# Kernel optimization log

Measured on AMD Instinct MI355X. Metric: run time of the kernel, lower is better.

Reference implementation:

```python
import jax, jax.numpy as jnp
import numpy as np
import math

FILTER_SIZE = 11
FILTER_SIGMA = 1.5
C1 = 0.01 ** 2
C2 = 0.03 ** 2
PAD = FILTER_SIZE // 2


def _make_gauss_kernel(sigma, kernel_size, channel=3):
    mean = np.floor(0.5 * kernel_size)
    x = np.arange(kernel_size, dtype=np.float64)
    k1d = np.exp(-((x - mean) ** 2) / (2 * sigma ** 2)) * (1.0 / (2 * math.pi * sigma ** 2))
    k2d = np.outer(k1d, k1d).astype(np.float32)
    k2d = k2d / k2d.sum()
    # OIHW depthwise kernel: [channel, 1, k, k]
    return np.broadcast_to(k2d[None, None], (channel, 1, kernel_size, kernel_size)).copy()


def _depthwise_blur(x, kernel):
    # x: [B, 3, H, W], kernel: [3, 1, k, k]; groups=3, SAME padding (k//2)
    return jax.lax.conv_general_dilated(
        x, kernel,
        window_strides=(1, 1),
        padding=[(PAD, PAD), (PAD, PAD)],
        dimension_numbers=('NCHW', 'OIHW', 'NCHW'),
        feature_group_count=3,
    )


def setup_inputs() -> dict:
    key = jax.random.key(0)
    k1, k2 = jax.random.split(key)
    B, C, H, W = 32, 3, 512, 512
    image1 = jax.random.uniform(k1, (B, C, H, W), dtype=jnp.float32)
    image2 = jax.random.uniform(k2, (B, C, H, W), dtype=jnp.float32)
    gauss_kernel = jnp.asarray(_make_gauss_kernel(FILTER_SIGMA, FILTER_SIZE, channel=3))
    return {"image1": image1, "image2": image2, "gauss_kernel": gauss_kernel}


def reference(image1, image2, gauss_kernel):
    mu1 = _depthwise_blur(image1, gauss_kernel)
    mu2 = _depthwise_blur(image2, gauss_kernel)
    mu1_sq = mu1 * mu1
    mu2_sq = mu2 * mu2
    mu1_mu2 = mu1 * mu2
    sig1_sq = _depthwise_blur(image1 * image1, gauss_kernel) - mu1_sq
    sig2_sq = _depthwise_blur(image2 * image2, gauss_kernel) - mu2_sq
    sig1_sig2 = _depthwise_blur(image1 * image2, gauss_kernel) - mu1_mu2
    ssim_num = (2.0 * mu1_mu2 + C1) * (2.0 * sig1_sig2 + C2)
    ssim_den = (mu1_sq + mu2_sq + C1) * (sig1_sq + sig2_sq + C2)
    ssim_map = ssim_num / ssim_den
    dssim_map = (1.0 - ssim_map) * 0.5
    return dssim_map.mean()  # size_average=True
```

## Files before the change

### kernel.cpp

```cpp
#include <hip/hip_runtime.h>
#include <math.h>


namespace {
constexpr int IMG = 512;
constexpr int TW = 32;
constexpr int RB = 64;
constexpr int RING = RB + 10;
constexpr int SLOT = 44;
constexpr int XGN = TW / 8;
constexpr int NCHUNK = IMG / RB;
constexpr int CTILES = IMG / TW;
constexpr int NIMG = 96;
constexpr float C1c = 1e-4f;
constexpr float C2c = 9e-4f;
constexpr float INV_N = 1.0f / 25165824.0f;
}

typedef float v2f __attribute__((ext_vector_type(2)));

__global__ void dssim_zero(float* ws) { ws[0] = 0.0f; }

__global__ void dssim_final(const float* __restrict__ ws, float* __restrict__ out) {
  out[0] = ws[0] * INV_N;
}

__global__ __launch_bounds__(256, 3) void dssim_main(
    const float* __restrict__ im1, const float* __restrict__ im2,
    const float* __restrict__ gk, float* __restrict__ ws)
{
  __shared__ float sR[XGN * RING * SLOT];

  const int tid = threadIdx.x;
  const int bid = blockIdx.x;
  const int img = bid >> 4;
  const int tsx = bid & 15;
  const int X0s = tsx * TW;

  const float* __restrict__ p1 = im1 + (size_t)img * (IMG * IMG);
  const float* __restrict__ p2 = im2 + (size_t)img * (IMG * IMG);

  float wt[11];
  {
    float ic = 1.0f / sqrtf(gk[5 * 11 + 5]);
    #pragma unroll
    for (int i = 0; i < 11; ++i) wt[i] = gk[i * 11 + 5] * ic;
  }
  v2f wp[12];
  #pragma unroll
  for (int m = 0; m < 12; ++m) {
    float lo = (m <= 10) ? wt[m] : 0.f;
    float hi = (m >= 1) ? wt[m - 1] : 0.f;
    wp[m].x = lo; wp[m].y = hi;
  }

  const int c   = tid & 31;
  const int yg  = tid >> 5;
  const int xg3 = c >> 3;
  const int cl  = c & 7;

  float lsum = 0.f;

  for (int k = 0; k < NCHUNK; ++k) {
    const int r0    = (k == 0) ? -5 : RB * k + 5;
    const int ntask = (k == 0) ? XGN * RING : XGN * RB;
    for (int t = tid; t < ntask; t += 256) {
      const int xg = t & 3, dr = t >> 2;
      const int r  = r0 + dr;
      const int rr = (r + 5) % RING;
      const int cb = X0s + xg * 8 - 8;

      float a24[24], b24[24];
      if ((unsigned)r < (unsigned)IMG) {
        const float* row1 = p1 + r * IMG;
        const float* row2 = p2 + r * IMG;
        if (cb >= 0 && cb + 24 <= IMG) {
          #pragma unroll
          for (int i = 0; i < 6; ++i) {
            float4 v1 = *(const float4*)(row1 + cb + 4 * i);
            float4 v2 = *(const float4*)(row2 + cb + 4 * i);
            a24[4*i+0] = v1.x; a24[4*i+1] = v1.y; a24[4*i+2] = v1.z; a24[4*i+3] = v1.w;
            b24[4*i+0] = v2.x; b24[4*i+1] = v2.y; b24[4*i+2] = v2.z; b24[4*i+3] = v2.w;
          }
        } else {
          #pragma unroll
          for (int e = 0; e < 24; ++e) {
            int cc = cb + e;
            bool ok = (unsigned)cc < (unsigned)IMG;
            a24[e] = ok ? row1[cc] : 0.f;
            b24[e] = ok ? row2[cc] : 0.f;
          }
        }
      } else {
        #pragma unroll
        for (int e = 0; e < 24; ++e) { a24[e] = 0.f; b24[e] = 0.f; }
      }

      v2f o0[4], o1[4], o2[4], o3[4], o4[4];
      #pragma unroll
      for (int jp = 0; jp < 4; ++jp) {
        o0[jp] = 0.f; o1[jp] = 0.f; o2[jp] = 0.f; o3[jp] = 0.f; o4[jp] = 0.f;
      }
      #pragma unroll
      for (int e = 0; e < 18; ++e) {
        float va = a24[e + 3], vb = b24[e + 3];
        float pa = va * va, pb = vb * vb, pab = va * vb;
        v2f va2; va2.x = va; va2.y = va;
        v2f vb2; vb2.x = vb; vb2.y = vb;
        v2f pa2; pa2.x = pa; pa2.y = pa;
        v2f pb2; pb2.x = pb; pb2.y = pb;
        v2f pc2; pc2.x = pab; pc2.y = pab;
        #pragma unroll
        for (int jp = 0; jp < 4; ++jp) {
          int m = e - 2 * jp;
          if (m >= 0 && m < 12) {
            v2f w = wp[m];
            o0[jp] = __builtin_elementwise_fma(w, va2, o0[jp]);
            o1[jp] = __builtin_elementwise_fma(w, vb2, o1[jp]);
            o2[jp] = __builtin_elementwise_fma(w, pa2, o2[jp]);
            o3[jp] = __builtin_elementwise_fma(w, pb2, o3[jp]);
            o4[jp] = __builtin_elementwise_fma(w, pc2, o4[jp]);
          }
        }
      }

      const int base = (xg * RING + rr) * SLOT;
      #pragma unroll
      for (int jp = 0; jp < 4; ++jp) {
        *(float4*)&sR[base + 8 * jp]     = make_float4(o0[jp].x, o1[jp].x, o2[jp].x, o3[jp].x);
        *(float4*)&sR[base + 8 * jp + 4] = make_float4(o0[jp].y, o1[jp].y, o2[jp].y, o3[jp].y);
      }
      *(float4*)&sR[base + 32] = make_float4(o4[0].x, o4[0].y, o4[1].x, o4[1].y);
      *(float4*)&sR[base + 36] = make_float4(o4[2].x, o4[2].y, o4[3].x, o4[3].y);
    }
    __syncthreads();

    v2f m1p[4], m2p[4], e11p[4], e22p[4], e12p[4];
    #pragma unroll
    for (int jp = 0; jp < 4; ++jp) {
      m1p[jp] = 0.f; m2p[jp] = 0.f; e11p[jp] = 0.f; e22p[jp] = 0.f; e12p[jp] = 0.f;
    }

    const int rbase = (RB * k + yg * 8) % RING;
    #pragma unroll
    for (int rr = 0; rr < 18; ++rr) {
      int idx = rbase + rr;
      if (idx >= RING) idx -= RING;
      const int a = (xg3 * RING + idx) * SLOT;
      float4 v4 = *(const float4*)&sR[a + 4 * cl];
      float  v5 = sR[a + 32 + cl];
      v2f x1; x1.x = v4.x; x1.y = v4.x;
      v2f x2; x2.x = v4.y; x2.y = v4.y;
      v2f x3; x3.x = v4.z; x3.y = v4.z;
      v2f x4; x4.x = v4.w; x4.y = v4.w;
      v2f x5; x5.x = v5;   x5.y = v5;
      #pragma unroll
      for (int jp = 0; jp < 4; ++jp) {
        int m = rr - 2 * jp;
        if (m >= 0 && m < 12) {
          v2f w = wp[m];
          m1p[jp]  = __builtin_elementwise_fma(w, x1, m1p[jp]);
          m2p[jp]  = __builtin_elementwise_fma(w, x2, m2p[jp]);
          e11p[jp] = __builtin_elementwise_fma(w, x3, e11p[jp]);
          e22p[jp] = __builtin_elementwise_fma(w, x4, e22p[jp]);
          e12p[jp] = __builtin_elementwise_fma(w, x5, e12p[jp]);
        }
      }
    }

    #pragma unroll
    for (int jp = 0; jp < 4; ++jp) {
      v2f m1 = m1p[jp], m2 = m2p[jp];
      v2f m1s = m1 * m1, m2s = m2 * m2, m12 = m1 * m2;
      v2f s11 = e11p[jp] - m1s, s22 = e22p[jp] - m2s, s12 = e12p[jp] - m12;
      v2f num = (2.f * m12 + C1c) * (2.f * s12 + C2c);
      v2f den = (m1s + m2s + C1c) * (s11 + s22 + C2c);
      lsum += (1.f - num.x * __builtin_amdgcn_rcpf(den.x)) * 0.5f;
      lsum += (1.f - num.y * __builtin_amdgcn_rcpf(den.y)) * 0.5f;
    }
    __syncthreads();
  }

  #pragma unroll
  for (int off = 32; off > 0; off >>= 1) lsum += __shfl_down(lsum, off);
  if ((tid & 63) == 0) atomicAdd(ws, lsum);
}

extern "C" void kernel_launch(void* const* d_in, const int* in_sizes, int n_in,
                              void* d_out, int out_size, void* d_ws, size_t ws_size,
                              hipStream_t stream) {
  const float* im1 = (const float*)d_in[0];
  const float* im2 = (const float*)d_in[1];
  const float* gk  = (const float*)d_in[2];
  float* out = (float*)d_out;
  float* ws  = (float*)d_ws;

  hipLaunchKernelGGL(dssim_zero, dim3(1), dim3(1), 0, stream, ws);
  hipLaunchKernelGGL(dssim_main, dim3(NIMG * CTILES), dim3(256), 0, stream,
                     im1, im2, gk, ws);
  hipLaunchKernelGGL(dssim_final, dim3(1), dim3(1), 0, stream, ws, out);
}
```

Baseline: 291.3 us.

## Split image rows into segments, shrink chunks and per-thread work for occupancy

Each block now covers one 128-row segment of a 32-column strip instead of the full image height, so the grid is four times larger. The chunk height drops from 64 to 32 rows, and each thread in the horizontal pass produces 4 columns instead of 8. The vertical pass now yields 4 outputs per thread instead of 8, and launch bounds rise to 5 blocks per SM. The per-block partial sums are also combined through shared memory so only one atomic is issued per block. The aim is more parallelism and occupancy through smaller register and LDS footprints, at the cost of recomputing the 10-row halo for every segment and loading overlapping input columns.

```diff
diff --git a/kernel.cpp b/kernel.cpp
--- a/kernel.cpp
+++ b/kernel.cpp
@@ -5,11 +5,13 @@
 namespace {
 constexpr int IMG = 512;
 constexpr int TW = 32;
-constexpr int RB = 64;
+constexpr int RB = 32;
 constexpr int RING = RB + 10;
 constexpr int SLOT = 44;
 constexpr int XGN = TW / 8;
-constexpr int NCHUNK = IMG / RB;
+constexpr int SEGR = 128;
+constexpr int NCHUNK = SEGR / RB;
+constexpr int SEGN = IMG / SEGR;
 constexpr int CTILES = IMG / TW;
 constexpr int NIMG = 96;
 constexpr float C1c = 1e-4f;
@@ -25,7 +27,7 @@
   out[0] = ws[0] * INV_N;
 }
 
-__global__ __launch_bounds__(256, 3) void dssim_main(
+__global__ __launch_bounds__(256, 5) void dssim_main(
     const float* __restrict__ im1, const float* __restrict__ im2,
     const float* __restrict__ gk, float* __restrict__ ws)
 {
@@ -33,9 +35,12 @@
 
   const int tid = threadIdx.x;
   const int bid = blockIdx.x;
-  const int img = bid >> 4;
-  const int tsx = bid & 15;
+  const int img = bid >> 6;
+  const int rem = bid & 63;
+  const int tsx = rem & 15;
+  const int seg = rem >> 4;
   const int X0s = tsx * TW;
+  const int Y0  = seg * SEGR;
 
   const float* __restrict__ p1 = im1 + (size_t)img * (IMG * IMG);
   const float* __restrict__ p2 = im2 + (size_t)img * (IMG * IMG);
@@ -61,91 +66,98 @@
 
   float lsum = 0.f;
 
-  for (int k = 0; k < NCHUNK; ++k) {
-    const int r0    = (k == 0) ? -5 : RB * k + 5;
-    const int ntask = (k == 0) ? XGN * RING : XGN * RB;
+  for (int kc = 0; kc < NCHUNK; ++kc) {
+    const int r0    = (kc == 0) ? -5 : RB * kc + 5;
+    const int ntask = (kc == 0) ? 8 * RING : 8 * RB;
     for (int t = tid; t < ntask; t += 256) {
-      const int xg = t & 3, dr = t >> 2;
-      const int r  = r0 + dr;
-      const int rr = (r + 5) % RING;
-      const int cb = X0s + xg * 8 - 8;
-
-      float a24[24], b24[24];
-      if ((unsigned)r < (unsigned)IMG) {
-        const float* row1 = p1 + r * IMG;
-        const float* row2 = p2 + r * IMG;
-        if (cb >= 0 && cb + 24 <= IMG) {
+      const int colsub = t & 7;
+      const int dr  = t >> 3;
+      const int rl  = r0 + dr;
+      const int ry  = Y0 + rl;
+      const int rr  = (rl + 5) % RING;
+      const int xg  = colsub >> 1;
+      const int sub = colsub & 1;
+      const int cbs = X0s + xg * 8 + sub * 4 - 8;
+
+      float a20[20], b20[20];
+      if ((unsigned)ry < (unsigned)IMG) {
+        const float* row1 = p1 + (size_t)ry * IMG;
+        const float* row2 = p2 + (size_t)ry * IMG;
+        if (cbs >= 0 && cbs + 20 <= IMG) {
           #pragma unroll
-          for (int i = 0; i < 6; ++i) {
-            float4 v1 = *(const float4*)(row1 + cb + 4 * i);
-            float4 v2 = *(const float4*)(row2 + cb + 4 * i);
-            a24[4*i+0] = v1.x; a24[4*i+1] = v1.y; a24[4*i+2] = v1.z; a24[4*i+3] = v1.w;
-            b24[4*i+0] = v2.x; b24[4*i+1] = v2.y; b24[4*i+2] = v2.z; b24[4*i+3] = v2.w;
+          for (int i = 0; i < 5; ++i) {
+            float4 v1 = *(const float4*)(row1 + cbs + 4 * i);
+            float4 v2 = *(const float4*)(row2 + cbs + 4 * i);
+            a20[4*i+0] = v1.x; a20[4*i+1] = v1.y; a20[4*i+2] = v1.z; a20[4*i+3] = v1.w;
+            b20[4*i+0] = v2.x; b20[4*i+1] = v2.y; b20[4*i+2] = v2.z; b20[4*i+3] = v2.w;
           }
         } else {
           #pragma unroll
-          for (int e = 0; e < 24; ++e) {
-            int cc = cb + e;
+          for (int e = 0; e < 20; ++e) {
+            int cc = cbs + e;
             bool ok = (unsigned)cc < (unsigned)IMG;
-            a24[e] = ok ? row1[cc] : 0.f;
-            b24[e] = ok ? row2[cc] : 0.f;
+            a20[e] = ok ? row1[cc] : 0.f;
+            b20[e] = ok ? row2[cc] : 0.f;
           }
         }
       } else {
         #pragma unroll
-        for (int e = 0; e < 24; ++e) { a24[e] = 0.f; b24[e] = 0.f; }
-      }
-
-      v2f o0[4], o1[4], o2[4], o3[4], o4[4];
+        for (int e = 0; e < 20; ++e) { a20[e] = 0.f; b20[e] = 0.f; }
+      }
+
+      v2f o0[2], o1[2], o2[2], o3[2], o4[2];
       #pragma unroll
-      for (int jp = 0; jp < 4; ++jp) {
+      for (int jp = 0; jp < 2; ++jp) {
         o0[jp] = 0.f; o1[jp] = 0.f; o2[jp] = 0.f; o3[jp] = 0.f; o4[jp] = 0.f;
       }
       #pragma unroll
-      for (int e = 0; e < 18; ++e) {
-        float va = a24[e + 3], vb = b24[e + 3];
+      for (int i = 3; i <= 16; ++i) {
+        float va = a20[i], vb = b20[i];
         float pa = va * va, pb = vb * vb, pab = va * vb;
         v2f va2; va2.x = va; va2.y = va;
         v2f vb2; vb2.x = vb; vb2.y = vb;
         v2f pa2; pa2.x = pa; pa2.y = pa;
         v2f pb2; pb2.x = pb; pb2.y = pb;
         v2f pc2; pc2.x = pab; pc2.y = pab;
-        #pragma unroll
-        for (int jp = 0; jp < 4; ++jp) {
-          int m = e - 2 * jp;
-          if (m >= 0 && m < 12) {
-            v2f w = wp[m];
-            o0[jp] = __builtin_elementwise_fma(w, va2, o0[jp]);
-            o1[jp] = __builtin_elementwise_fma(w, vb2, o1[jp]);
-            o2[jp] = __builtin_elementwise_fma(w, pa2, o2[jp]);
-            o3[jp] = __builtin_elementwise_fma(w, pb2, o3[jp]);
-            o4[jp] = __builtin_elementwise_fma(w, pc2, o4[jp]);
-          }
+        if (i - 3 < 12) {
+          v2f w = wp[i - 3];
+          o0[0] = __builtin_elementwise_fma(w, va2, o0[0]);
+          o1[0] = __builtin_elementwise_fma(w, vb2, o1[0]);
+          o2[0] = __builtin_elementwise_fma(w, pa2, o2[0]);
+          o3[0] = __builtin_elementwise_fma(w, pb2, o3[0]);
+          o4[0] = __builtin_elementwise_fma(w, pc2, o4[0]);
         }
-      }
-
-      const int base = (xg * RING + rr) * SLOT;
-      #pragma unroll
-      for (int jp = 0; jp < 4; ++jp) {
-        *(float4*)&sR[base + 8 * jp]     = make_float4(o0[jp].x, o1[jp].x, o2[jp].x, o3[jp].x);
-        *(float4*)&sR[base + 8 * jp + 4] = make_float4(o0[jp].y, o1[jp].y, o2[jp].y, o3[jp].y);
-      }
-      *(float4*)&sR[base + 32] = make_float4(o4[0].x, o4[0].y, o4[1].x, o4[1].y);
-      *(float4*)&sR[base + 36] = make_float4(o4[2].x, o4[2].y, o4[3].x, o4[3].y);
+        if (i - 5 >= 0) {
+          v2f w = wp[i - 5];
+          o0[1] = __builtin_elementwise_fma(w, va2, o0[1]);
+          o1[1] = __builtin_elementwise_fma(w, vb2, o1[1]);
+          o2[1] = __builtin_elementwise_fma(w, pa2, o2[1]);
+          o3[1] = __builtin_elementwise_fma(w, pb2, o3[1]);
+          o4[1] = __builtin_elementwise_fma(w, pc2, o4[1]);
+        }
+      }
+
+      const int base  = (xg * RING + rr) * SLOT;
+      const int jbase = base + 16 * sub;
+      *(float4*)&sR[jbase]      = make_float4(o0[0].x, o1[0].x, o2[0].x, o3[0].x);
+      *(float4*)&sR[jbase + 4]  = make_float4(o0[0].y, o1[0].y, o2[0].y, o3[0].y);
+      *(float4*)&sR[jbase + 8]  = make_float4(o0[1].x, o1[1].x, o2[1].x, o3[1].x);
+      *(float4*)&sR[jbase + 12] = make_float4(o0[1].y, o1[1].y, o2[1].y, o3[1].y);
+      *(float4*)&sR[base + 32 + 4 * sub] =
+          make_float4(o4[0].x, o4[0].y, o4[1].x, o4[1].y);
     }
     __syncthreads();
 
-    v2f m1p[4], m2p[4], e11p[4], e22p[4], e12p[4];
-    #pragma unroll
-    for (int jp = 0; jp < 4; ++jp) {
+    v2f m1p[2], m2p[2], e11p[2], e22p[2], e12p[2];
+    #pragma unroll
+    for (int jp = 0; jp < 2; ++jp) {
       m1p[jp] = 0.f; m2p[jp] = 0.f; e11p[jp] = 0.f; e22p[jp] = 0.f; e12p[jp] = 0.f;
     }
 
-    const int rbase = (RB * k + yg * 8) % RING;
-    #pragma unroll
-    for (int rr = 0; rr < 18; ++rr) {
-      int idx = rbase + rr;
-      if (idx >= RING) idx -= RING;
+    const int y0l = RB * kc + yg * 4;
+    int idx = y0l % RING;
+    #pragma unroll
+    for (int rr = 0; rr < 14; ++rr) {
       const int a = (xg3 * RING + idx) * SLOT;
       float4 v4 = *(const float4*)&sR[a + 4 * cl];
       float  v5 = sR[a + 32 + cl];
@@ -154,22 +166,27 @@
       v2f x3; x3.x = v4.z; x3.y = v4.z;
       v2f x4; x4.x = v4.w; x4.y = v4.w;
       v2f x5; x5.x = v5;   x5.y = v5;
-      #pragma unroll
-      for (int jp = 0; jp < 4; ++jp) {
-        int m = rr - 2 * jp;
-        if (m >= 0 && m < 12) {
-          v2f w = wp[m];
-          m1p[jp]  = __builtin_elementwise_fma(w, x1, m1p[jp]);
-          m2p[jp]  = __builtin_elementwise_fma(w, x2, m2p[jp]);
-          e11p[jp] = __builtin_elementwise_fma(w, x3, e11p[jp]);
-          e22p[jp] = __builtin_elementwise_fma(w, x4, e22p[jp]);
-          e12p[jp] = __builtin_elementwise_fma(w, x5, e12p[jp]);
-        }
-      }
-    }
-
-    #pragma unroll
-    for (int jp = 0; jp < 4; ++jp) {
+      if (rr < 12) {
+        v2f w = wp[rr];
+        m1p[0]  = __builtin_elementwise_fma(w, x1, m1p[0]);
+        m2p[0]  = __builtin_elementwise_fma(w, x2, m2p[0]);
+        e11p[0] = __builtin_elementwise_fma(w, x3, e11p[0]);
+        e22p[0] = __builtin_elementwise_fma(w, x4, e22p[0]);
+        e12p[0] = __builtin_elementwise_fma(w, x5, e12p[0]);
+      }
+      if (rr >= 2) {
+        v2f w = wp[rr - 2];
+        m1p[1]  = __builtin_elementwise_fma(w, x1, m1p[1]);
+        m2p[1]  = __builtin_elementwise_fma(w, x2, m2p[1]);
+        e11p[1] = __builtin_elementwise_fma(w, x3, e11p[1]);
+        e22p[1] = __builtin_elementwise_fma(w, x4, e22p[1]);
+        e12p[1] = __builtin_elementwise_fma(w, x5, e12p[1]);
+      }
+      idx++; if (idx == RING) idx = 0;
+    }
+
+    #pragma unroll
+    for (int jp = 0; jp < 2; ++jp) {
       v2f m1 = m1p[jp], m2 = m2p[jp];
       v2f m1s = m1 * m1, m2s = m2 * m2, m12 = m1 * m2;
       v2f s11 = e11p[jp] - m1s, s22 = e22p[jp] - m2s, s12 = e12p[jp] - m12;
@@ -183,7 +200,9 @@
 
   #pragma unroll
   for (int off = 32; off > 0; off >>= 1) lsum += __shfl_down(lsum, off);
-  if ((tid & 63) == 0) atomicAdd(ws, lsum);
+  if ((tid & 63) == 0) sR[tid >> 6] = lsum;
+  __syncthreads();
+  if (tid == 0) atomicAdd(ws, sR[0] + sR[1] + sR[2] + sR[3]);
 }
 
 extern "C" void kernel_launch(void* const* d_in, const int* in_sizes, int n_in,
@@ -196,7 +215,7 @@
   float* ws  = (float*)d_ws;
 
   hipLaunchKernelGGL(dssim_zero, dim3(1), dim3(1), 0, stream, ws);
-  hipLaunchKernelGGL(dssim_main, dim3(NIMG * CTILES), dim3(256), 0, stream,
+  hipLaunchKernelGGL(dssim_main, dim3(NIMG * CTILES * SEGN), dim3(256), 0, stream,
                      im1, im2, gk, ws);
   hipLaunchKernelGGL(dssim_final, dim3(1), dim3(1), 0, stream, ws, out);
 }
```

Result: slower. 309.2 us (+6.1%).

## Merge squared-sum blurs, split rows into segments, swizzle LDS ring slots

Applied to the files above, without the earlier changes.

Since SSIM only needs sigma1^2+sigma2^2, the a^2 and b^2 blurs are merged into one blur of a^2+b^2, cutting the blurred quantities from five to four. This shrinks the LDS slot to 32 floats and the FMA count in both blur passes. Image rows are split into four 128-row segments per block, giving four times more blocks with halo rows recomputed at segment edges. LDS offsets are rotated to reduce bank conflicts, launch bounds are raised to 4 blocks per CU, and per-block partial sums are combined in LDS so each block does one atomic. The merged sum can lose some float precision.

```diff
diff --git a/kernel.cpp b/kernel.cpp
--- a/kernel.cpp
+++ b/kernel.cpp
@@ -7,9 +7,11 @@
 constexpr int TW = 32;
 constexpr int RB = 64;
 constexpr int RING = RB + 10;
-constexpr int SLOT = 44;
+constexpr int SLOT = 32;
 constexpr int XGN = TW / 8;
-constexpr int NCHUNK = IMG / RB;
+constexpr int SEGR = 128;
+constexpr int NCHUNK = SEGR / RB;
+constexpr int SEGN = IMG / SEGR;
 constexpr int CTILES = IMG / TW;
 constexpr int NIMG = 96;
 constexpr float C1c = 1e-4f;
@@ -25,7 +27,7 @@
   out[0] = ws[0] * INV_N;
 }
 
-__global__ __launch_bounds__(256, 3) void dssim_main(
+__global__ __launch_bounds__(256, 4) void dssim_main(
     const float* __restrict__ im1, const float* __restrict__ im2,
     const float* __restrict__ gk, float* __restrict__ ws)
 {
@@ -33,9 +35,12 @@
 
   const int tid = threadIdx.x;
   const int bid = blockIdx.x;
-  const int img = bid >> 4;
-  const int tsx = bid & 15;
+  const int img = bid >> 6;
+  const int rem = bid & 63;
+  const int tsx = rem & 15;
+  const int seg = rem >> 4;
   const int X0s = tsx * TW;
+  const int Y0  = seg * SEGR;
 
   const float* __restrict__ p1 = im1 + (size_t)img * (IMG * IMG);
   const float* __restrict__ p2 = im2 + (size_t)img * (IMG * IMG);
@@ -61,19 +66,20 @@
 
   float lsum = 0.f;
 
-  for (int k = 0; k < NCHUNK; ++k) {
-    const int r0    = (k == 0) ? -5 : RB * k + 5;
-    const int ntask = (k == 0) ? XGN * RING : XGN * RB;
+  for (int kc = 0; kc < NCHUNK; ++kc) {
+    const int r0    = (kc == 0) ? -5 : RB * kc + 5;
+    const int ntask = (kc == 0) ? XGN * RING : XGN * RB;
     for (int t = tid; t < ntask; t += 256) {
       const int xg = t & 3, dr = t >> 2;
-      const int r  = r0 + dr;
-      const int rr = (r + 5) % RING;
+      const int rl = r0 + dr;
+      const int ry = Y0 + rl;
+      const int rr = (rl + 5) % RING;
       const int cb = X0s + xg * 8 - 8;
 
       float a24[24], b24[24];
-      if ((unsigned)r < (unsigned)IMG) {
-        const float* row1 = p1 + r * IMG;
-        const float* row2 = p2 + r * IMG;
+      if ((unsigned)ry < (unsigned)IMG) {
+        const float* row1 = p1 + (size_t)ry * IMG;
+        const float* row2 = p2 + (size_t)ry * IMG;
         if (cb >= 0 && cb + 24 <= IMG) {
           #pragma unroll
           for (int i = 0; i < 6; ++i) {
@@ -96,20 +102,20 @@
         for (int e = 0; e < 24; ++e) { a24[e] = 0.f; b24[e] = 0.f; }
       }
 
-      v2f o0[4], o1[4], o2[4], o3[4], o4[4];
+      v2f o0[4], o1[4], oS[4], oX[4];
       #pragma unroll
       for (int jp = 0; jp < 4; ++jp) {
-        o0[jp] = 0.f; o1[jp] = 0.f; o2[jp] = 0.f; o3[jp] = 0.f; o4[jp] = 0.f;
+        o0[jp] = 0.f; o1[jp] = 0.f; oS[jp] = 0.f; oX[jp] = 0.f;
       }
       #pragma unroll
       for (int e = 0; e < 18; ++e) {
         float va = a24[e + 3], vb = b24[e + 3];
-        float pa = va * va, pb = vb * vb, pab = va * vb;
+        float px = va * vb;
+        float ps = va * va + vb * vb;
         v2f va2; va2.x = va; va2.y = va;
         v2f vb2; vb2.x = vb; vb2.y = vb;
-        v2f pa2; pa2.x = pa; pa2.y = pa;
-        v2f pb2; pb2.x = pb; pb2.y = pb;
-        v2f pc2; pc2.x = pab; pc2.y = pab;
+        v2f ps2; ps2.x = ps; ps2.y = ps;
+        v2f px2; px2.x = px; px2.y = px;
         #pragma unroll
         for (int jp = 0; jp < 4; ++jp) {
           int m = e - 2 * jp;
@@ -117,64 +123,63 @@
             v2f w = wp[m];
             o0[jp] = __builtin_elementwise_fma(w, va2, o0[jp]);
             o1[jp] = __builtin_elementwise_fma(w, vb2, o1[jp]);
-            o2[jp] = __builtin_elementwise_fma(w, pa2, o2[jp]);
-            o3[jp] = __builtin_elementwise_fma(w, pb2, o3[jp]);
-            o4[jp] = __builtin_elementwise_fma(w, pc2, o4[jp]);
+            oS[jp] = __builtin_elementwise_fma(w, ps2, oS[jp]);
+            oX[jp] = __builtin_elementwise_fma(w, px2, oX[jp]);
           }
         }
       }
 
       const int base = (xg * RING + rr) * SLOT;
+      const int rot  = 4 * (rr & 7) + 8 * xg;
       #pragma unroll
       for (int jp = 0; jp < 4; ++jp) {
-        *(float4*)&sR[base + 8 * jp]     = make_float4(o0[jp].x, o1[jp].x, o2[jp].x, o3[jp].x);
-        *(float4*)&sR[base + 8 * jp + 4] = make_float4(o0[jp].y, o1[jp].y, o2[jp].y, o3[jp].y);
-      }
-      *(float4*)&sR[base + 32] = make_float4(o4[0].x, o4[0].y, o4[1].x, o4[1].y);
-      *(float4*)&sR[base + 36] = make_float4(o4[2].x, o4[2].y, o4[3].x, o4[3].y);
+        *(float4*)&sR[base + ((4 * (2 * jp) + rot) & 31)] =
+            make_float4(o0[jp].x, o1[jp].x, oS[jp].x, oX[jp].x);
+        *(float4*)&sR[base + ((4 * (2 * jp + 1) + rot) & 31)] =
+            make_float4(o0[jp].y, o1[jp].y, oS[jp].y, oX[jp].y);
+      }
     }
     __syncthreads();
 
-    v2f m1p[4], m2p[4], e11p[4], e22p[4], e12p[4];
+    v2f m1p[4], m2p[4], eSp[4], eXp[4];
     #pragma unroll
     for (int jp = 0; jp < 4; ++jp) {
-      m1p[jp] = 0.f; m2p[jp] = 0.f; e11p[jp] = 0.f; e22p[jp] = 0.f; e12p[jp] = 0.f;
-    }
-
-    const int rbase = (RB * k + yg * 8) % RING;
+      m1p[jp] = 0.f; m2p[jp] = 0.f; eSp[jp] = 0.f; eXp[jp] = 0.f;
+    }
+
+    const int y0l = RB * kc + yg * 8;
+    int idx = y0l % RING;
     #pragma unroll
     for (int rr = 0; rr < 18; ++rr) {
-      int idx = rbase + rr;
-      if (idx >= RING) idx -= RING;
-      const int a = (xg3 * RING + idx) * SLOT;
-      float4 v4 = *(const float4*)&sR[a + 4 * cl];
-      float  v5 = sR[a + 32 + cl];
+      const int a = (xg3 * RING + idx) * SLOT +
+                    ((4 * cl + 4 * (idx & 7) + 8 * xg3) & 31);
+      float4 v4 = *(const float4*)&sR[a];
       v2f x1; x1.x = v4.x; x1.y = v4.x;
       v2f x2; x2.x = v4.y; x2.y = v4.y;
       v2f x3; x3.x = v4.z; x3.y = v4.z;
       v2f x4; x4.x = v4.w; x4.y = v4.w;
-      v2f x5; x5.x = v5;   x5.y = v5;
       #pragma unroll
       for (int jp = 0; jp < 4; ++jp) {
         int m = rr - 2 * jp;
         if (m >= 0 && m < 12) {
           v2f w = wp[m];
-          m1p[jp]  = __builtin_elementwise_fma(w, x1, m1p[jp]);
-          m2p[jp]  = __builtin_elementwise_fma(w, x2, m2p[jp]);
-          e11p[jp] = __builtin_elementwise_fma(w, x3, e11p[jp]);
-          e22p[jp] = __builtin_elementwise_fma(w, x4, e22p[jp]);
-          e12p[jp] = __builtin_elementwise_fma(w, x5, e12p[jp]);
+          m1p[jp] = __builtin_elementwise_fma(w, x1, m1p[jp]);
+          m2p[jp] = __builtin_elementwise_fma(w, x2, m2p[jp]);
+          eSp[jp] = __builtin_elementwise_fma(w, x3, eSp[jp]);
+          eXp[jp] = __builtin_elementwise_fma(w, x4, eXp[jp]);
         }
       }
+      idx++; if (idx == RING) idx = 0;
     }
 
     #pragma unroll
     for (int jp = 0; jp < 4; ++jp) {
       v2f m1 = m1p[jp], m2 = m2p[jp];
       v2f m1s = m1 * m1, m2s = m2 * m2, m12 = m1 * m2;
-      v2f s11 = e11p[jp] - m1s, s22 = e22p[jp] - m2s, s12 = e12p[jp] - m12;
+      v2f sS  = eSp[jp] - m1s - m2s;
+      v2f s12 = eXp[jp] - m12;
       v2f num = (2.f * m12 + C1c) * (2.f * s12 + C2c);
-      v2f den = (m1s + m2s + C1c) * (s11 + s22 + C2c);
+      v2f den = (m1s + m2s + C1c) * (sS + C2c);
       lsum += (1.f - num.x * __builtin_amdgcn_rcpf(den.x)) * 0.5f;
       lsum += (1.f - num.y * __builtin_amdgcn_rcpf(den.y)) * 0.5f;
     }
@@ -183,7 +188,9 @@
 
   #pragma unroll
   for (int off = 32; off > 0; off >>= 1) lsum += __shfl_down(lsum, off);
-  if ((tid & 63) == 0) atomicAdd(ws, lsum);
+  if ((tid & 63) == 0) sR[tid >> 6] = lsum;
+  __syncthreads();
+  if (tid == 0) atomicAdd(ws, sR[0] + sR[1] + sR[2] + sR[3]);
 }
 
 extern "C" void kernel_launch(void* const* d_in, const int* in_sizes, int n_in,
@@ -196,7 +203,7 @@
   float* ws  = (float*)d_ws;
 
   hipLaunchKernelGGL(dssim_zero, dim3(1), dim3(1), 0, stream, ws);
-  hipLaunchKernelGGL(dssim_main, dim3(NIMG * CTILES), dim3(256), 0, stream,
+  hipLaunchKernelGGL(dssim_main, dim3(NIMG * CTILES * SEGN), dim3(256), 0, stream,
                      im1, im2, gk, ws);
   hipLaunchKernelGGL(dssim_final, dim3(1), dim3(1), 0, stream, ws, out);
 }
```

Measured after the change: 270.1 us. -7.3%, faster.
